# Kernel optimization log

Hardware: AMD Instinct MI355X
Metric: run time of the kernel (lower is better)

## Reference

```python
import jax, jax.numpy as jnp
import numpy as np

M, N = 512, 768

def setup_inputs() -> dict:
    key = jax.random.key(0)
    k1, _ = jax.random.split(key)
    repr_ = jax.random.normal(k1, (M, N), dtype=jnp.float32)
    GT = jnp.arange(M, dtype=jnp.int64)
    return {"repr": repr_, "GT": GT}

def reference(repr, GT):
    # Reorder features by ground-truth order: r[k] = repr[GT[k]]
    r = repr[GT]                                  # [M, N]
    # All pairwise differences r_i - r_j, clamped at 0 (relu)
    diff = jnp.maximum(r[:, None, :] - r[None, :, :], 0.0)   # [M, M, N]
    sumsq = jnp.sum(diff * diff, axis=-1)          # [M, M]
    # Only pairs with i < j in GT order contribute
    m = r.shape[0]
    mask = jnp.triu(jnp.ones((m, m), dtype=bool), k=1)
    # Guard sqrt at masked (zero) entries for numerical safety
    norms = jnp.sqrt(jnp.where(mask, sumsq, 1.0))
    return jnp.sum(jnp.where(mask, norms, 0.0))
```

## Files before the change

### kernel.cpp

```cpp
#include <hip/hip_runtime.h>


#define NN 768
#define TT 64
#define NTILE 36
#define NSPLIT 48
#define NC 16
#define SJ 20
#define PPT 4096

__global__ __launch_bounds__(256, 4)
void ClipPairWiseLossAll_partial(const float* __restrict__ repr,
                                 const int* __restrict__ GT,
                                 float* __restrict__ ws) {
    __shared__ float lds[128 * SJ];

    const int b     = blockIdx.x;
    const int tile  = b % NTILE;
    const int chunk = b / NTILE;
    int tj = 0;
    while (((tj + 1) * (tj + 2)) >> 1 <= tile) tj++;
    const int ti = tile - ((tj * (tj + 1)) >> 1);
    const int ibase = ti * TT;
    const int jbase = tj * TT;
    const int c0    = chunk * NC;

    const int t  = threadIdx.x;
    const int tx = t & 15;
    const int ty = t >> 4;

    const int sg = t & 3;
    const int sr = t >> 2;
    const int ri = GT[ibase + sr];
    const int rj = GT[jbase + sr];
    const float4 vI = *(const float4*)(repr + (size_t)ri * NN + c0 + (sg << 2));
    const float4 vJ = *(const float4*)(repr + (size_t)rj * NN + c0 + (sg << 2));
    *(float4*)(lds + sr * SJ + (sg << 2)) = vI;
    *(float4*)(lds + (TT + sr) * SJ + (sg << 2)) = vJ;
    __syncthreads();

    float acc[4][4] = {{0.f}};
#pragma unroll
    for (int g = 0; g < NC / 4; g++) {
        float4 vi[4], vj[4];
#pragma unroll
        for (int m = 0; m < 4; m++)
            vi[m] = *(const float4*)(lds + (ty + (m << 4)) * SJ + (g << 2));
#pragma unroll
        for (int k = 0; k < 4; k++)
            vj[k] = *(const float4*)(lds + (TT + tx + (k << 4)) * SJ + (g << 2));
#pragma unroll
        for (int m = 0; m < 4; m++) {
#pragma unroll
            for (int k = 0; k < 4; k++) {
                float d, a = acc[m][k];
                d = fmaxf(vi[m].x - vj[k].x, 0.f); a = fmaf(d, d, a);
                d = fmaxf(vi[m].y - vj[k].y, 0.f); a = fmaf(d, d, a);
                d = fmaxf(vi[m].z - vj[k].z, 0.f); a = fmaf(d, d, a);
                d = fmaxf(vi[m].w - vj[k].w, 0.f); a = fmaf(d, d, a);
                acc[m][k] = a;
            }
        }
    }

    float* wp = ws + (size_t)tile * PPT;
#pragma unroll
    for (int m = 0; m < 4; m++)
#pragma unroll
        for (int k = 0; k < 4; k++)
            atomicAdd(&wp[(ty + (m << 4)) * TT + (tx + (k << 4))], acc[m][k]);
}

__global__ __launch_bounds__(256)
void ClipPairWiseLossAll_finish(const float* __restrict__ ws,
                                float* __restrict__ out) {
    __shared__ float red[4];
    const int t    = threadIdx.x;
    const int tile = blockIdx.x;
    int tj = 0;
    while (((tj + 1) * (tj + 2)) >> 1 <= tile) tj++;
    const int ti = tile - ((tj * (tj + 1)) >> 1);
    const int ibase = ti * TT;
    const int jbase = tj * TT;

    const float* base = ws + (size_t)tile * PPT;
    float val = 0.f;
#pragma unroll
    for (int k = 0; k < 4; k++) {
        const int q  = t + (k << 8);
        const int iy = q >> 4;
        const int jx = (q & 15) << 2;
        const float4 s = *(const float4*)(base + (q << 2));
        const int gi = ibase + iy;
        const int gj = jbase + jx;
        if (gi < gj)     val += sqrtf(s.x);
        if (gi < gj + 1) val += sqrtf(s.y);
        if (gi < gj + 2) val += sqrtf(s.z);
        if (gi < gj + 3) val += sqrtf(s.w);
    }
#pragma unroll
    for (int off = 32; off > 0; off >>= 1)
        val += __shfl_down(val, off, 64);
    const int lane = t & 63, w = t >> 6;
    if (lane == 0) red[w] = val;
    __syncthreads();
    if (t == 0) atomicAdd(out, red[0] + red[1] + red[2] + red[3]);
}

extern "C" void kernel_launch(void* const* d_in, const int* in_sizes, int n_in,
                              void* d_out, int out_size, void* d_ws, size_t ws_size,
                              hipStream_t stream) {
    const float* repr = (const float*)d_in[0];
    const int*   GT   = (const int*)d_in[1];
    float* out = (float*)d_out;
    float* ws  = (float*)d_ws;

    ClipPairWiseLossAll_partial<<<NTILE * NSPLIT, 256, 0, stream>>>(repr, GT, ws);
    ClipPairWiseLossAll_finish<<<NTILE, 256, 0, stream>>>(ws, out);
}
```

Before: 82.79 us.

## Replace atomic partial accumulation with per-chunk workspace slabs and wider column chunks

Each block now processes 64 feature columns instead of 16, so there are 12 splits instead of 48. Each block writes its 4x4 partial sums straight to its own workspace slab with float4 stores, replacing the global atomics. The finish kernel runs four blocks per tile, sums the 12 slabs and applies the upper-triangular mask before the sqrt. This removes the atomic contention and the zero-initialization dependency on the workspace, at the cost of more workspace memory, fewer blocks in flight and a longer inner loop per block.

```diff
diff --git a/kernel.cpp b/kernel.cpp
--- a/kernel.cpp
+++ b/kernel.cpp
@@ -4,9 +4,9 @@
 #define NN 768
 #define TT 64
 #define NTILE 36
-#define NSPLIT 48
-#define NC 16
-#define SJ 20
+#define NSPLIT 12
+#define NC 64
+#define SJ 68
 #define PPT 4096
 
 __global__ __launch_bounds__(256, 4)
@@ -29,18 +29,24 @@
     const int tx = t & 15;
     const int ty = t >> 4;
 
-    const int sg = t & 3;
-    const int sr = t >> 2;
-    const int ri = GT[ibase + sr];
-    const int rj = GT[jbase + sr];
-    const float4 vI = *(const float4*)(repr + (size_t)ri * NN + c0 + (sg << 2));
-    const float4 vJ = *(const float4*)(repr + (size_t)rj * NN + c0 + (sg << 2));
-    *(float4*)(lds + sr * SJ + (sg << 2)) = vI;
-    *(float4*)(lds + (TT + sr) * SJ + (sg << 2)) = vJ;
+    const int sg = t & 15;
+    const int sr = t >> 4;
+    int rowidx[8];
+#pragma unroll
+    for (int k = 0; k < 8; k++) {
+        const int r = sr + (k << 4);
+        rowidx[k] = (r < TT) ? GT[ibase + r] : GT[jbase + (r - TT)];
+    }
+#pragma unroll
+    for (int k = 0; k < 8; k++) {
+        const int r = sr + (k << 4);
+        const float4 v = *(const float4*)(repr + (size_t)rowidx[k] * NN + c0 + (sg << 2));
+        *(float4*)(lds + r * SJ + (sg << 2)) = v;
+    }
     __syncthreads();
 
     float acc[4][4] = {{0.f}};
-#pragma unroll
+#pragma unroll 2
     for (int g = 0; g < NC / 4; g++) {
         float4 vi[4], vj[4];
 #pragma unroll
@@ -63,12 +69,13 @@
         }
     }
 
-    float* wp = ws + (size_t)tile * PPT;
+    float* wp = ws + ((size_t)tile * NSPLIT + chunk) * PPT;
 #pragma unroll
-    for (int m = 0; m < 4; m++)
-#pragma unroll
-        for (int k = 0; k < 4; k++)
-            atomicAdd(&wp[(ty + (m << 4)) * TT + (tx + (k << 4))], acc[m][k]);
+    for (int m = 0; m < 4; m++) {
+        float4 st;
+        st.x = acc[m][0]; st.y = acc[m][1]; st.z = acc[m][2]; st.w = acc[m][3];
+        *(float4*)(wp + (m << 10) + (t << 2)) = st;
+    }
 }
 
 __global__ __launch_bounds__(256)
@@ -76,28 +83,32 @@
                                 float* __restrict__ out) {
     __shared__ float red[4];
     const int t    = threadIdx.x;
-    const int tile = blockIdx.x;
+    const int tile = blockIdx.x >> 2;
+    const int m    = blockIdx.x & 3;
     int tj = 0;
     while (((tj + 1) * (tj + 2)) >> 1 <= tile) tj++;
     const int ti = tile - ((tj * (tj + 1)) >> 1);
     const int ibase = ti * TT;
     const int jbase = tj * TT;
 
-    const float* base = ws + (size_t)tile * PPT;
+    const float* base = ws + (size_t)tile * (NSPLIT * PPT) + (m << 10) + (t << 2);
+    float4 s; s.x = 0.f; s.y = 0.f; s.z = 0.f; s.w = 0.f;
+#pragma unroll
+    for (int c = 0; c < NSPLIT; c++) {
+        const float4 v = *(const float4*)(base + c * PPT);
+        s.x += v.x; s.y += v.y; s.z += v.z; s.w += v.w;
+    }
+
+    const int iy = (t >> 4) + (m << 4);
+    const int jx = (t & 15);
+    const int gi = ibase + iy;
+    const int gj = jbase + jx;
     float val = 0.f;
-#pragma unroll
-    for (int k = 0; k < 4; k++) {
-        const int q  = t + (k << 8);
-        const int iy = q >> 4;
-        const int jx = (q & 15) << 2;
-        const float4 s = *(const float4*)(base + (q << 2));
-        const int gi = ibase + iy;
-        const int gj = jbase + jx;
-        if (gi < gj)     val += sqrtf(s.x);
-        if (gi < gj + 1) val += sqrtf(s.y);
-        if (gi < gj + 2) val += sqrtf(s.z);
-        if (gi < gj + 3) val += sqrtf(s.w);
-    }
+    if (gi < gj)      val += sqrtf(s.x);
+    if (gi < gj + 16) val += sqrtf(s.y);
+    if (gi < gj + 32) val += sqrtf(s.z);
+    if (gi < gj + 48) val += sqrtf(s.w);
+
 #pragma unroll
     for (int off = 32; off > 0; off >>= 1)
         val += __shfl_down(val, off, 64);
@@ -116,5 +127,5 @@
     float* ws  = (float*)d_ws;
 
     ClipPairWiseLossAll_partial<<<NTILE * NSPLIT, 256, 0, stream>>>(repr, GT, ws);
-    ClipPairWiseLossAll_finish<<<NTILE, 256, 0, stream>>>(ws, out);
+    ClipPairWiseLossAll_finish<<<NTILE * 4, 256, 0, stream>>>(ws, out);
 }
```

Result: faster. 72.56 us (-12.4%).
